# Performance work log

Measured on AMD Instinct MI355X. Metric: run time of the kernel, lower is better.

Reference implementation:

```python
import jax, jax.numpy as jnp
import numpy as np
import math

B, DIM, H, W = 4, 96, 64, 64
DIM3 = DIM * 3
DSTATE = 16

def _dwconv(x, w, b):
    # x: (B, d, L); torch Conv1d(k=4, pad=3, groups=d) then slice [:L] == left-pad 3
    y = jax.lax.conv_general_dilated(x, w, (1,), [(3, 0)],
                                     dimension_numbers=('NCH', 'OIH', 'NCH'),
                                     feature_group_count=x.shape[1])
    return y + b[None, :, None]

def _ln(x, g, b):
    m = jnp.mean(x, -1, keepdims=True)
    v = jnp.var(x, -1, keepdims=True)
    return (x - m) * jax.lax.rsqrt(v + 1e-5) * g + b

def _selective_scan(u, delta, A, Bs, Cs, D, z, delta_bias):
    # u, delta, z: (B, d, L); A: (d, N); Bs, Cs: (B, N, L)
    delta = jax.nn.softplus(delta + delta_bias[None, :, None])
    dT, uT = jnp.moveaxis(delta, 2, 0), jnp.moveaxis(u, 2, 0)   # (L, B, d)
    BT, CT = jnp.moveaxis(Bs, 2, 0), jnp.moveaxis(Cs, 2, 0)     # (L, B, N)
    h0 = jnp.zeros((u.shape[0], A.shape[0], A.shape[1]), u.dtype)
    def step(h, inp):
        d_t, u_t, b_t, c_t = inp
        h = jnp.exp(d_t[..., None] * A) * h + (d_t * u_t)[..., None] * b_t[:, None, :]
        return h, jnp.einsum('bdn,bn->bd', h, c_t)
    _, ys = jax.lax.scan(step, h0, (dT, uT, BT, CT))
    y = jnp.moveaxis(ys, 0, 2) + D[None, :, None] * u
    return y * jax.nn.silu(z)

def _sss(x, z_anchor, in_w, conv_w, conv_b, x_w, dt_w, dt_b, Alog, Dp, out_w):
    Bb, C, Hh, Ww = x.shape
    L = Hh * Ww
    r = dt_w.shape[0]
    xf = x.reshape(Bb, C, L).transpose(0, 2, 1) + z_anchor[:, None, :]
    x_in, z_gate = jnp.split(xf @ in_w, 2, axis=-1)
    xc = jax.nn.silu(_dwconv(x_in.transpose(0, 2, 1), conv_w, conv_b))  # (B, di, L)
    xdbl = xc.transpose(0, 2, 1) @ x_w
    dt, Bs, Cs = jnp.split(xdbl, [r, r + DSTATE], axis=-1)
    y = _selective_scan(xc, (dt @ dt_w).transpose(0, 2, 1), -jnp.exp(Alog),
                        Bs.transpose(0, 2, 1), Cs.transpose(0, 2, 1), Dp,
                        z_gate.transpose(0, 2, 1), dt_b)
    return (y.transpose(0, 2, 1) @ out_w).transpose(0, 2, 1).reshape(Bb, C, Hh, Ww)

def _sts(x, K, Q, in_w, conv_w, conv_b, kln_g, kln_b, k_w, k_b, qln_g, qln_b, q_w, q_b,
         dtbc_w, dt_w, dt_b, gate_w, gate_b, Alog, Dp, out_w):
    Bb, C, Hh, Ww = x.shape
    L = Hh * Ww
    r = dt_w.shape[0]
    xf = x.reshape(Bb, C, L).transpose(0, 2, 1)
    xc = jax.nn.silu(_dwconv((xf @ in_w).transpose(0, 2, 1), conv_w, conv_b))  # (B, di, L)
    x_t = xc.transpose(0, 2, 1)
    Kf = K.reshape(Bb, C, L).transpose(0, 2, 1)
    Qf = Q.reshape(Bb, C, L).transpose(0, 2, 1)
    K_p = jax.nn.silu(_ln(Kf, kln_g, kln_b) @ k_w + k_b)
    Q_p = jax.nn.silu(_ln(Qf, qln_g, qln_b) @ q_w + q_b)
    xdbl = jnp.concatenate([x_t, K_p], -1) @ dtbc_w
    dt, Bs, Cs = jnp.split(xdbl, [r, r + DSTATE], axis=-1)
    z_g = (jnp.concatenate([x_t, Q_p], -1) @ gate_w + gate_b).transpose(0, 2, 1)
    y = _selective_scan(xc, (dt @ dt_w).transpose(0, 2, 1), -jnp.exp(Alog),
                        Bs.transpose(0, 2, 1), Cs.transpose(0, 2, 1), Dp, z_g, dt_b)
    return (y.transpose(0, 2, 1) @ out_w).transpose(0, 2, 1).reshape(Bb, C, Hh, Ww)

def setup_inputs():
    key = jax.random.key(0)
    ks = iter(jax.random.split(key, 64))
    def nrm(shape, s=0.02):
        return jax.random.normal(next(ks), shape, jnp.float32) * s
    di, di3 = DIM * 2, DIM3 * 2
    r, r3 = math.ceil(DIM / 16), math.ceil(DIM3 / 16)
    Alog = jnp.log(jnp.tile(jnp.arange(1.0, DSTATE + 1.0, dtype=jnp.float32), (di, 1)))
    Alog3 = jnp.log(jnp.tile(jnp.arange(1.0, DSTATE + 1.0, dtype=jnp.float32), (di3, 1)))
    return dict(
        m_ll=jax.random.normal(next(ks), (B, DIM, H, W), jnp.float32),
        m_high=jax.random.normal(next(ks), (B, DIM3, H, W), jnp.float32),
        z=jax.random.normal(next(ks), (B, DIM), jnp.float32),
        K=jax.random.normal(next(ks), (B, DIM3, H, W), jnp.float32),
        Q=jax.random.normal(next(ks), (B, DIM3, H, W), jnp.float32),
        s_in_w=nrm((DIM, 2 * di)), s_conv_w=nrm((di, 1, 4), 0.2), s_conv_b=nrm((di,)),
        s_x_w=nrm((di, r + 2 * DSTATE)), s_dt_w=nrm((r, di)), s_dt_b=nrm((di,)),
        s_Alog=Alog, s_D=jnp.ones((di,), jnp.float32), s_out_w=nrm((di, DIM)),
        t_in_w=nrm((DIM3, di3)), t_conv_w=nrm((di3, 1, 4), 0.2), t_conv_b=nrm((di3,)),
        t_kln_g=jnp.ones((DIM3,), jnp.float32), t_kln_b=jnp.zeros((DIM3,), jnp.float32),
        t_k_w=nrm((DIM3, di3)), t_k_b=nrm((di3,)),
        t_qln_g=jnp.ones((DIM3,), jnp.float32), t_qln_b=jnp.zeros((DIM3,), jnp.float32),
        t_q_w=nrm((DIM3, di3)), t_q_b=nrm((di3,)),
        t_dtbc_w=nrm((2 * di3, r3 + 2 * DSTATE)), t_dt_w=nrm((r3, di3)), t_dt_b=nrm((di3,)),
        t_gate_w=nrm((2 * di3, di3)), t_gate_b=nrm((di3,)),
        t_Alog=Alog3, t_D=jnp.ones((di3,), jnp.float32), t_out_w=nrm((di3, DIM3)),
    )

def reference(m_ll, m_high, z, K, Q,
              s_in_w, s_conv_w, s_conv_b, s_x_w, s_dt_w, s_dt_b, s_Alog, s_D, s_out_w,
              t_in_w, t_conv_w, t_conv_b, t_kln_g, t_kln_b, t_k_w, t_k_b,
              t_qln_g, t_qln_b, t_q_w, t_q_b, t_dtbc_w, t_dt_w, t_dt_b,
              t_gate_w, t_gate_b, t_Alog, t_D, t_out_w):
    o1 = m_ll + _sss(m_ll, z, s_in_w, s_conv_w, s_conv_b, s_x_w, s_dt_w, s_dt_b, s_Alog, s_D, s_out_w)
    o2 = m_high + _sts(m_high, K, Q, t_in_w, t_conv_w, t_conv_b, t_kln_g, t_kln_b, t_k_w, t_k_b,
                       t_qln_g, t_qln_b, t_q_w, t_q_b, t_dtbc_w, t_dt_w, t_dt_b,
                       t_gate_w, t_gate_b, t_Alog, t_D, t_out_w)
    return (o1, o2)
```

## Files before the change

### kernel.cpp

```cpp
#include <hip/hip_runtime.h>
#include <math.h>

#define L 4096

typedef unsigned short u16;
typedef unsigned int u32;
typedef float f32x4 __attribute__((ext_vector_type(4)));
typedef short s16x8 __attribute__((ext_vector_type(8)));
typedef __attribute__((address_space(3))) unsigned int lds_u32;
typedef __attribute__((address_space(1))) unsigned int glb_u32;

__device__ __forceinline__ float softplus_f(float x) {
  return fmaxf(x, 0.f) + log1pf(__expf(-fabsf(x)));
}
__device__ __forceinline__ float silu_f(float x) {
  return x / (1.f + __expf(-x));
}
__device__ __forceinline__ float bf2f(u16 v) {
  return __uint_as_float(((unsigned)v) << 16);
}
__device__ __forceinline__ u16 f2bf(float f) {
  unsigned u = __float_as_uint(f);
  u += 0x7FFFu + ((u >> 16) & 1u);
  return (u16)(u >> 16);
}

struct WSeg { const float* src; u16* dst; int K, N, Npad; };
struct WAll { WSeg s[8]; };

__global__ __launch_bounds__(256) void wconv_k(WAll wa) {
  const WSeg w = wa.s[blockIdx.z];
  const int nb = blockIdx.x * 32, kb = blockIdx.y * 32;
  if (nb >= w.Npad || kb >= w.K) return;
  __shared__ float t[32][33];
  const int tx = threadIdx.x & 31, ty = threadIdx.x >> 5;
  for (int r = ty; r < 32; r += 8) {
    int k = kb + r, n = nb + tx;
    t[r][tx] = (n < w.N) ? w.src[(size_t)k * w.N + n] : 0.f;
  }
  __syncthreads();
  for (int r = ty; r < 32; r += 8) {
    int n = nb + r;
    w.dst[(size_t)n * w.K + kb + tx] = f2bf(t[tx][r]);
  }
}

struct TSeg { const float *x, *gam, *bet, *bias2; u16* out; int C, doLN; };
struct TPack { TSeg s[4]; };

__global__ __launch_bounds__(256) void trans_pack_k(TPack pk) {
  const TSeg t = pk.s[blockIdx.x >> 9];
  const int local = blockIdx.x & 511;
  const int C = t.C;
  __shared__ float tile[288][33];
  __shared__ float psum[8][32], psq[8][32];
  __shared__ float mm[32], rr[32];
  const int tid = threadIdx.x;
  const int l0 = (local & 127) * 32;
  const int b = local >> 7;
  const int lane32 = tid & 31, row8 = tid >> 5;
  const float* xb = t.x + (size_t)b * C * L + l0;

  for (int c = row8; c < C; c += 8)
    tile[c][lane32] = xb[(size_t)c * L + lane32];
  __syncthreads();

  if (t.doLN) {
    float s = 0.f, sq = 0.f;
    for (int c = row8; c < C; c += 8) {
      float v = tile[c][lane32];
      s += v; sq = fmaf(v, v, sq);
    }
    psum[row8][lane32] = s; psq[row8][lane32] = sq;
    __syncthreads();
    if (row8 == 0) {
      float ts = 0.f, tq = 0.f;
      #pragma unroll
      for (int g = 0; g < 8; ++g) { ts += psum[g][lane32]; tq += psq[g][lane32]; }
      float m = ts / C;
      float var = tq / C - m * m;
      mm[lane32] = m;
      rr[lane32] = rsqrtf(var + 1e-5f);
    }
    __syncthreads();
  }

  u16* ob = t.out + ((size_t)b * L + l0) * C;
  const int total = 32 * C;
  for (int o = tid * 8; o < total; o += 2048) {
    int tt = o / C, c = o % C;
    float m = 0.f, rs = 0.f;
    if (t.doLN) { m = mm[tt]; rs = rr[tt]; }
    union { u16 u[8]; int4 v; } pkv;
    #pragma unroll
    for (int j = 0; j < 8; ++j) {
      float v = tile[c + j][tt];
      if (t.doLN) v = (v - m) * rs * t.gam[c + j] + t.bet[c + j];
      else if (t.bias2) v += t.bias2[b * C + c + j];
      pkv.u[j] = f2bf(v);
    }
    *(int4*)(ob + o) = pkv.v;
  }
}

struct CSeg { const u16* x; const float* w; const float* b; u16* y; int C, nbx; };
struct CPack { CSeg s[2]; int start1; };

__global__ __launch_bounds__(256) void conv_pack_k(CPack pk) {
  const int bid = blockIdx.x;
  const int si = bid >= pk.start1;
  const CSeg q = pk.s[si];
  const int local = si ? bid - pk.start1 : bid;
  const int C = q.C;
  const int c = (local % q.nbx) * 64 + (threadIdx.x & 63);
  const int chunk = (local / q.nbx) * 4 + (threadIdx.x >> 6);
  const int T0 = chunk * 8;
  const float w0 = q.w[c * 4], w1 = q.w[c * 4 + 1], w2 = q.w[c * 4 + 2], w3 = q.w[c * 4 + 3];
  const float bs = q.b[c];
  const bool first = (T0 & (L - 1)) == 0;
  float v[11];
  #pragma unroll
  for (int i = 0; i < 11; ++i) {
    if (i < 3 && first) v[i] = 0.f;
    else v[i] = bf2f(q.x[(size_t)(T0 - 3 + i) * C + c]);
  }
  #pragma unroll
  for (int j = 0; j < 8; ++j) {
    float s = bs + w0 * v[j] + w1 * v[j + 1] + w2 * v[j + 2] + w3 * v[j + 3];
    q.y[(size_t)(T0 + j) * C + c] = f2bf(silu_f(s));
  }
}

struct MSeg {
  const u16 *A0, *A1, *Wt;
  const float *bias, *res;
  float* outF; u16 *outB0, *outB1;
  int K, K1, Nout, ldA, ldo, split, nbx, nwg, epi;
};
struct MPack { MSeg s[4]; int starts[4]; int nseg; };

__global__ __launch_bounds__(256) void mfma_pack_k(MPack pk) {
  const int bid = blockIdx.x;
  int si = 0;
  #pragma unroll
  for (int k = 1; k < 4; ++k)
    if (k < pk.nseg && bid >= pk.starts[k]) si = k;
  const MSeg p = pk.s[si];
  const int wg = bid - pk.starts[si];

  __shared__ u16 lds[16384];
  u16* As0 = lds;
  u16* Bs0 = lds + 8192;
  const int tid = threadIdx.x;
  const int lane = tid & 63;
  const int wid = tid >> 6;
  const int wm = wid >> 1, wn = wid & 1;
  const int newid = (wg & 7) * (p.nwg >> 3) + (wg >> 3);
  const int n0 = (newid % p.nbx) * 128;
  const int m0 = (newid / p.nbx) * 128;
  const int srow = tid & 127;
  const int skc = tid >> 7;
  const int kgrp = lane >> 4, l16 = lane & 15;

  f32x4 acc[4][4];
  #pragma unroll
  for (int i = 0; i < 4; ++i)
    #pragma unroll
    for (int j = 0; j < 4; ++j)
      acc[i][j] = (f32x4){0.f, 0.f, 0.f, 0.f};

  auto stage = [&](int bi, int k0) {
    const u16* Ab = p.A0;
    int kc = k0;
    if (p.A1 && k0 >= p.K1) { Ab = p.A1; kc = k0 - p.K1; }
    const u16* g0 = Ab + (size_t)(m0 + srow) * p.ldA + kc + skc * 8;
    u16* Ad = As0 + bi * 4096;
    __builtin_amdgcn_global_load_lds((const glb_u32*)g0,
        (lds_u32*)(Ad + wid * 512), 16, 0, 0);
    __builtin_amdgcn_global_load_lds((const glb_u32*)(g0 + 16),
        (lds_u32*)(Ad + 2048 + wid * 512), 16, 0, 0);
    const u16* h0 = p.Wt + (size_t)(n0 + srow) * p.K + k0 + skc * 8;
    u16* Bd = Bs0 + bi * 4096;
    __builtin_amdgcn_global_load_lds((const glb_u32*)h0,
        (lds_u32*)(Bd + wid * 512), 16, 0, 0);
    __builtin_amdgcn_global_load_lds((const glb_u32*)(h0 + 16),
        (lds_u32*)(Bd + 2048 + wid * 512), 16, 0, 0);
  };

  const int nt = p.K >> 5;
  stage(0, 0);
  __syncthreads();
  for (int t = 0; t < nt; ++t) {
    const int cur = t & 1;
    if (t + 1 < nt) stage(cur ^ 1, (t + 1) << 5);
    s16x8 af[4], bfr[4];
    #pragma unroll
    for (int mi = 0; mi < 4; ++mi)
      af[mi] = *(const s16x8*)(As0 + cur * 4096 + kgrp * 1024 + (wm * 64 + mi * 16 + l16) * 8);
    #pragma unroll
    for (int ni = 0; ni < 4; ++ni)
      bfr[ni] = *(const s16x8*)(Bs0 + cur * 4096 + kgrp * 1024 + (wn * 64 + ni * 16 + l16) * 8);
    #pragma unroll
    for (int mi = 0; mi < 4; ++mi)
      #pragma unroll
      for (int ni = 0; ni < 4; ++ni)
        acc[mi][ni] = __builtin_amdgcn_mfma_f32_16x16x32_bf16(af[mi], bfr[ni], acc[mi][ni], 0, 0, 0);
    if (t + 1 < nt) __syncthreads();
  }

  if (p.epi == 0) {
    #pragma unroll
    for (int mi = 0; mi < 4; ++mi) {
      #pragma unroll
      for (int j = 0; j < 4; ++j) {
        int token = m0 + wm * 64 + mi * 16 + (lane >> 4) * 4 + j;
        #pragma unroll
        for (int ni = 0; ni < 4; ++ni) {
          int n = n0 + wn * 64 + ni * 16 + l16;
          if (n < p.Nout) p.outF[(size_t)token * p.ldo + n] = acc[mi][ni][j];
        }
      }
    }
  } else if (p.epi == 2) {
    #pragma unroll
    for (int mi = 0; mi < 4; ++mi) {
      int token = m0 + wm * 64 + mi * 16 + (lane >> 4) * 4;
      int b = token >> 12, l = token & (L - 1);
      #pragma unroll
      for (int ni = 0; ni < 4; ++ni) {
        int n = n0 + wn * 64 + ni * 16 + l16;
        if (n < p.Nout) {
          size_t o = ((size_t)b * p.Nout + n) * L + l;
          float4 r = *(const float4*)(p.res + o);
          float4 v = make_float4(acc[mi][ni][0] + r.x, acc[mi][ni][1] + r.y,
                                 acc[mi][ni][2] + r.z, acc[mi][ni][3] + r.w);
          *(float4*)(p.outF + o) = v;
        }
      }
    }
  } else {
    __syncthreads();
    #pragma unroll
    for (int mi = 0; mi < 4; ++mi) {
      #pragma unroll
      for (int j = 0; j < 4; ++j) {
        int tok = wm * 64 + mi * 16 + (lane >> 4) * 4 + j;
        #pragma unroll
        for (int ni = 0; ni < 4; ++ni) {
          int nl = wn * 64 + ni * 16 + l16;
          int n = n0 + nl;
          float v = acc[mi][ni][j];
          if (n < p.Nout && (p.epi == 3 || p.epi == 4)) {
            v += p.bias[n];
            if (p.epi == 3) v = silu_f(v);
          }
          lds[tok * 128 + ((((nl >> 4) ^ (tok & 7))) << 4) + (nl & 15)] = f2bf(v);
        }
      }
    }
    __syncthreads();
    #pragma unroll
    for (int it = 0; it < 8; ++it) {
      int idx = it * 256 + tid;
      int row = idx >> 4, c16 = idx & 15;
      int nl0 = c16 * 8;
      if (n0 + nl0 < p.Nout) {
        int g = nl0 >> 4;
        int4 vv = *(const int4*)(lds + row * 128 + ((g ^ (row & 7)) << 4) + (nl0 & 15));
        int token = m0 + row;
        if (p.epi == 5) {
          int n = n0 + nl0;
          if (n < p.split) *(int4*)(p.outB0 + (size_t)token * p.split + n) = vv;
          else *(int4*)(p.outB1 + (size_t)token * p.split + (n - p.split)) = vv;
        } else {
          *(int4*)(p.outB0 + (size_t)token * p.ldo + n0 + nl0) = vv;
        }
      }
    }
  }
}

struct FSeg { const float* A0; const float* W; const float* eb; float* out; int K, N, lda, ldo, nbx; };
struct FPack { FSeg s[2]; int start1; };

__global__ __launch_bounds__(256) void gemm_f32_pack_k(FPack pk) {
  const int bid = blockIdx.x;
  const int si = bid >= pk.start1;
  const FSeg p = pk.s[si];
  const int local = si ? bid - pk.start1 : bid;
  const int n0 = (local % p.nbx) * 64;
  const int m0 = (local / p.nbx) * 64;

  __shared__ __align__(16) float As[16][64];
  __shared__ __align__(16) float Bs[16][64];
  const int tid = threadIdx.x;
  const int kidx = tid >> 4;
  const int li4 = (tid & 15) << 2;
  const int r0 = (tid & 15) << 2;
  const int c0 = (tid >> 4) << 2;
  float acc[4][4] = {};

  for (int k0 = 0; k0 < p.K; k0 += 16) {
    __syncthreads();
    {
      const int row = tid >> 2;
      const int kk4 = (tid & 3) << 2;
      const float* src = p.A0 + (size_t)(m0 + row) * p.lda;
      #pragma unroll
      for (int j = 0; j < 4; ++j) {
        int k = k0 + kk4 + j;
        As[kk4 + j][row] = (k < p.K) ? src[k] : 0.f;
      }
    }
    {
      int k = k0 + kidx;
      #pragma unroll
      for (int j = 0; j < 4; ++j) {
        int n = n0 + li4 + j;
        Bs[kidx][li4 + j] = (k < p.K && n < p.N) ? p.W[(size_t)k * p.N + n] : 0.f;
      }
    }
    __syncthreads();
    #pragma unroll
    for (int kk = 0; kk < 16; ++kk) {
      float4 a = *(const float4*)&As[kk][r0];
      float4 bq = *(const float4*)&Bs[kk][c0];
      float av[4] = {a.x, a.y, a.z, a.w};
      float bv[4] = {bq.x, bq.y, bq.z, bq.w};
      #pragma unroll
      for (int i = 0; i < 4; ++i)
        #pragma unroll
        for (int j = 0; j < 4; ++j)
          acc[i][j] = fmaf(av[i], bv[j], acc[i][j]);
    }
  }
  float eb[4] = {p.eb[n0 + c0], p.eb[n0 + c0 + 1], p.eb[n0 + c0 + 2], p.eb[n0 + c0 + 3]};
  #pragma unroll
  for (int i = 0; i < 4; ++i) {
    float4 v;
    v.x = softplus_f(acc[i][0] + eb[0]);
    v.y = softplus_f(acc[i][1] + eb[1]);
    v.z = softplus_f(acc[i][2] + eb[2]);
    v.w = softplus_f(acc[i][3] + eb[3]);
    *(float4*)&p.out[(size_t)(m0 + r0 + i) * p.ldo + n0 + c0] = v;
  }
}

struct S3Seg {
  const u16* u; const float* dlt; const float* Alog; const float* xdbl;
  const float* Dp; const u16* zT; float* PF; float* PF2; u16* yT;
  int roff, Dch, CLen, NCH, nsl, cSplit;
};
struct S3Pack { S3Seg s[2]; int start1; };

template<int PASS>
__global__ __launch_bounds__(256) void scan3_pack_k(S3Pack pk) {
  __shared__ float rows[64][32];
  const int bid = blockIdx.x;
  const int si = bid >= pk.start1;
  const S3Seg q = pk.s[si];
  const int local = si ? bid - pk.start1 : bid;
  const int nsl = q.nsl;
  const int NC = L / q.CLen;
  const int slice = local % nsl;
  const int c = (local / nsl) % NC;
  const int b = local / (nsl * NC);
  const int tid = threadIdx.x;
  const size_t tok0 = (size_t)b * L + (size_t)c * q.CLen;

  float* PFb;
  int cc;
  if (c < q.cSplit) { PFb = q.PF; cc = c; }
  else { PFb = q.PF2; cc = c - q.cSplit; }

  const int W2 = (PASS == 1) ? 8 : 16;
  const int tot2 = q.CLen * W2;
  for (int i = tid; i < tot2; i += 256) {
    int r = i / W2, j = i - r * W2;
    float2 v = *(const float2*)(q.xdbl + (tok0 + r) * 64 + q.roff + 2 * j);
    *(float2*)&rows[r][2 * j] = v;
  }
  __syncthreads();

  if (tid < 192) {
    const int d = slice * 192 + tid;
    const int Dch = q.Dch;
    float An[16], h[16];
    #pragma unroll
    for (int n = 0; n < 16; ++n) {
      An[n] = -__expf(q.Alog[d * 16 + n]);
      h[n] = 0.f;
    }
    bool fast = true;
    #pragma unroll
    for (int n = 1; n < 16; ++n) {
      float ref = (float)(n + 1) * An[0];
      if (fabsf(An[n] - ref) > 1e-4f * fabsf(ref)) fast = false;
    }
    const int ch = b * Dch + d;
    if (PASS == 3) {
      #pragma unroll
      for (int n = 0; n < 16; ++n)
        h[n] = PFb[((size_t)cc * 32 + 16 + n) * q.NCH + ch];
    }
    const float Dd = q.Dp[d];
    const u16* up = q.u + tok0 * Dch + d;
    const float* dp = q.dlt + tok0 * Dch + d;
    const u16* zp = q.zT + tok0 * Dch + d;
    u16* yr = q.yT + tok0 * Dch + d;
    float S = 0.f;

    #define SCAN_BODY(FAST)                                                    \
    for (int t = 0; t < q.CLen; ++t) {                                         \
      const size_t od = (size_t)t * Dch;                                       \
      float dl = dp[od];                                                       \
      float uu = bf2f(up[od]);                                                 \
      float w = dl * uu;                                                       \
      f32x4 B4[4];                                                             \
      _Pragma("unroll")                                                        \
      for (int g = 0; g < 4; ++g) B4[g] = *(const f32x4*)&rows[t][4 * g];      \
      if (PASS == 1) S += dl;                                                  \
      float y = 0.f;                                                           \
      if (FAST) {                                                              \
        float a = __expf(dl * An[0]);                                          \
        float e = a;                                                           \
        h[0] = fmaf(e, h[0], w * B4[0][0]);                                    \
        _Pragma("unroll")                                                      \
        for (int n = 1; n < 16; ++n) {                                         \
          e *= a;                                                              \
          h[n] = fmaf(e, h[n], w * B4[n >> 2][n & 3]);                         \
        }                                                                      \
      } else {                                                                 \
        _Pragma("unroll")                                                      \
        for (int n = 0; n < 16; ++n)                                           \
          h[n] = fmaf(__expf(dl * An[n]), h[n], w * B4[n >> 2][n & 3]);        \
      }                                                                        \
      if (PASS == 3) {                                                         \
        f32x4 C4[4];                                                           \
        _Pragma("unroll")                                                      \
        for (int g = 0; g < 4; ++g) C4[g] = *(const f32x4*)&rows[t][16 + 4 * g]; \
        _Pragma("unroll")                                                      \
        for (int n = 0; n < 16; ++n)                                           \
          y = fmaf(h[n], C4[n >> 2][n & 3], y);                                \
        float zv = bf2f(zp[od]);                                               \
        yr[od] = f2bf((y + Dd * uu) * silu_f(zv));                             \
      }                                                                        \
    }

    if (fast) { SCAN_BODY(1) } else { SCAN_BODY(0) }
    #undef SCAN_BODY

    if (PASS == 1) {
      #pragma unroll
      for (int n = 0; n < 16; ++n) {
        PFb[((size_t)cc * 32 + n) * q.NCH + ch] = __expf(An[n] * S);
        PFb[((size_t)cc * 32 + 16 + n) * q.NCH + ch] = h[n];
      }
    }
  }
}

__global__ __launch_bounds__(256) void stitch_pack_k(
    float* PA0, float* PB0, int sp0, int NC0, int NCH0, int tot0,
    float* PA1, float* PB1, int sp1, int NC1, int NCH1, int tot1) {
  int idx = blockIdx.x * 256 + threadIdx.x;
  float *PA, *PB; int sp, NC, NCH;
  if (idx < tot0) { PA = PA0; PB = PB0; sp = sp0; NC = NC0; NCH = NCH0; }
  else { idx -= tot0; if (idx >= tot1) return; PA = PA1; PB = PB1; sp = sp1; NC = NC1; NCH = NCH1; }
  int ch = idx % NCH, n = idx / NCH;
  float hin = 0.f;
  for (int c = 0; c < NC; ++c) {
    float* base = (c < sp) ? PA : PB;
    int cc = (c < sp) ? c : c - sp;
    float* Ps = base + ((size_t)cc * 32 + n) * NCH + ch;
    float* Fs = base + ((size_t)cc * 32 + 16 + n) * NCH + ch;
    float Pv = *Ps, Fv = *Fs;
    *Fs = hin;
    hin = fmaf(Pv, hin, Fv);
  }
}

extern "C" void kernel_launch(void* const* d_in, const int* in_sizes, int n_in,
                              void* d_out, int out_size, void* d_ws, size_t ws_size,
                              hipStream_t stream) {
  const float* m_ll    = (const float*)d_in[0];
  const float* m_high  = (const float*)d_in[1];
  const float* zanc    = (const float*)d_in[2];
  const float* Kin     = (const float*)d_in[3];
  const float* Qin     = (const float*)d_in[4];
  const float* s_in_w  = (const float*)d_in[5];
  const float* s_conv_w= (const float*)d_in[6];
  const float* s_conv_b= (const float*)d_in[7];
  const float* s_x_w   = (const float*)d_in[8];
  const float* s_dt_w  = (const float*)d_in[9];
  const float* s_dt_b  = (const float*)d_in[10];
  const float* s_Alog  = (const float*)d_in[11];
  const float* s_D     = (const float*)d_in[12];
  const float* s_out_w = (const float*)d_in[13];
  const float* t_in_w  = (const float*)d_in[14];
  const float* t_conv_w= (const float*)d_in[15];
  const float* t_conv_b= (const float*)d_in[16];
  const float* t_kln_g = (const float*)d_in[17];
  const float* t_kln_b = (const float*)d_in[18];
  const float* t_k_w   = (const float*)d_in[19];
  const float* t_k_b   = (const float*)d_in[20];
  const float* t_qln_g = (const float*)d_in[21];
  const float* t_qln_b = (const float*)d_in[22];
  const float* t_q_w   = (const float*)d_in[23];
  const float* t_q_b   = (const float*)d_in[24];
  const float* t_dtbc_w= (const float*)d_in[25];
  const float* t_dt_w  = (const float*)d_in[26];
  const float* t_dt_b  = (const float*)d_in[27];
  const float* t_gate_w= (const float*)d_in[28];
  const float* t_gate_b= (const float*)d_in[29];
  const float* t_Alog  = (const float*)d_in[30];
  const float* t_D     = (const float*)d_in[31];
  const float* t_out_w = (const float*)d_in[32];

  float* out1 = (float*)d_out;
  float* out2 = out1 + (size_t)4 * 96 * L;
  float* ws = (float*)d_ws;

  u16* w_sin   = (u16*)(ws + 0);
  u16* w_sx    = (u16*)(ws + 18432);
  u16* w_sout  = (u16*)(ws + 30720);
  u16* w_tin   = (u16*)(ws + 43008);
  u16* w_tk    = (u16*)(ws + 135168);
  u16* w_tq    = (u16*)(ws + 227328);
  u16* w_tdtbc = (u16*)(ws + 319488);
  u16* w_tgate = (u16*)(ws + 393216);
  u16* w_tout  = (u16*)(ws + 761856);

  float* B_ahi  = ws + 872448;
  float* B_aK   = ws + 3231744;
  float* B_aQ   = ws + 5591040;
  float* B_all  = ws + 7950336;
  float* B_xin  = ws + 8736768;
  float* B_zTs  = ws + 10309632;
  float* B_xc   = ws + 11882496;
  float* B_xin3 = ws + 13455360;
  float* B_xc3  = ws + 18173952;
  float* B_kp   = ws + 22892544;
  float* B_qp   = ws + 27611136;
  float* B_zg3  = ws + 32329728;
  float* B_xdbl = ws + 37048320;
  float* B_xdbl3= ws + 38096896;
  float* B_PFs  = ws + 39145472;
  float* B_dlt  = B_ahi;
  float* B_dlt3 = B_kp;
  u16* y_bf = (u16*)B_xin;
  u16* y3   = (u16*)B_xin3;
  float* PFt_a = out2;
  float* PFt_b = ws + 4018176;

  dim3 blk(256);

  {
    WAll wa;
    wa.s[0] = {s_in_w,   w_sin,    96, 384, 384};
    wa.s[1] = {s_x_w,    w_sx,    192,  38, 128};
    wa.s[2] = {s_out_w,  w_sout,  192,  96, 128};
    wa.s[3] = {t_in_w,   w_tin,   288, 576, 640};
    wa.s[4] = {t_k_w,    w_tk,    288, 576, 640};
    wa.s[5] = {t_q_w,    w_tq,    288, 576, 640};
    wa.s[6] = {t_dtbc_w, w_tdtbc, 1152, 50, 128};
    wa.s[7] = {t_gate_w, w_tgate, 1152, 576, 640};
    wconv_k<<<dim3(20, 36, 8), blk, 0, stream>>>(wa);
    WAll wb;
    wb.s[0] = {t_out_w,  w_tout,  576, 288, 384};
    wconv_k<<<dim3(12, 18, 1), blk, 0, stream>>>(wb);
  }

  {
    TPack tp{};
    tp.s[0] = {m_ll,   nullptr, nullptr, zanc,    (u16*)B_all, 96,  0};
    tp.s[1] = {m_high, nullptr, nullptr, nullptr, (u16*)B_ahi, 288, 0};
    tp.s[2] = {Kin,    t_kln_g, t_kln_b, nullptr, (u16*)B_aK,  288, 1};
    tp.s[3] = {Qin,    t_qln_g, t_qln_b, nullptr, (u16*)B_aQ,  288, 1};
    trans_pack_k<<<dim3(2048), blk, 0, stream>>>(tp);
  }

  {
    MPack pk{}; pk.nseg = 4;
    pk.starts[0] = 0; pk.starts[1] = 384; pk.starts[2] = 1024; pk.starts[3] = 1664;
    MSeg a{}; a.A0 = (u16*)B_all; a.Wt = w_sin; a.K = 96; a.K1 = 1 << 28; a.Nout = 384;
    a.ldA = 96; a.split = 192; a.outB0 = (u16*)B_xin; a.outB1 = (u16*)B_zTs;
    a.nbx = 3; a.nwg = 384; a.epi = 5; pk.s[0] = a;
    MSeg b{}; b.A0 = (u16*)B_ahi; b.Wt = w_tin; b.K = 288; b.K1 = 1 << 28; b.Nout = 576;
    b.ldA = 288; b.ldo = 576; b.outB0 = (u16*)B_xin3; b.nbx = 5; b.nwg = 640; b.epi = 1; pk.s[1] = b;
    MSeg c{}; c.A0 = (u16*)B_aK; c.Wt = w_tk; c.K = 288; c.K1 = 1 << 28; c.Nout = 576;
    c.ldA = 288; c.ldo = 576; c.bias = t_k_b; c.outB0 = (u16*)B_kp; c.nbx = 5; c.nwg = 640; c.epi = 3; pk.s[2] = c;
    MSeg d{}; d.A0 = (u16*)B_aQ; d.Wt = w_tq; d.K = 288; d.K1 = 1 << 28; d.Nout = 576;
    d.ldA = 288; d.ldo = 576; d.bias = t_q_b; d.outB0 = (u16*)B_qp; d.nbx = 5; d.nwg = 640; d.epi = 3; pk.s[3] = d;
    mfma_pack_k<<<dim3(2304), blk, 0, stream>>>(pk);
  }

  {
    CPack cp{}; cp.start1 = 1536;
    cp.s[0] = {(u16*)B_xin,  s_conv_w, s_conv_b, (u16*)B_xc,  192, 3};
    cp.s[1] = {(u16*)B_xin3, t_conv_w, t_conv_b, (u16*)B_xc3, 576, 9};
    conv_pack_k<<<dim3(6144), blk, 0, stream>>>(cp);
  }

  {
    MPack pk{}; pk.nseg = 3;
    pk.starts[0] = 0; pk.starts[1] = 128; pk.starts[2] = 256; pk.starts[3] = 896;
    MSeg a{}; a.A0 = (u16*)B_xc; a.Wt = w_sx; a.K = 192; a.K1 = 1 << 28; a.Nout = 64;
    a.ldA = 192; a.ldo = 64; a.outF = B_xdbl; a.nbx = 1; a.nwg = 128; a.epi = 0; pk.s[0] = a;
    MSeg b{}; b.A0 = (u16*)B_xc3; b.A1 = (u16*)B_kp; b.Wt = w_tdtbc; b.K = 1152; b.K1 = 576;
    b.Nout = 64; b.ldA = 576; b.ldo = 64; b.outF = B_xdbl3; b.nbx = 1; b.nwg = 128; b.epi = 0; pk.s[1] = b;
    MSeg c{}; c.A0 = (u16*)B_xc3; c.A1 = (u16*)B_qp; c.Wt = w_tgate; c.K = 1152; c.K1 = 576;
    c.Nout = 576; c.ldA = 576; c.ldo = 576; c.bias = t_gate_b; c.outB0 = (u16*)B_zg3;
    c.nbx = 5; c.nwg = 640; c.epi = 4; pk.s[2] = c;
    mfma_pack_k<<<dim3(896), blk, 0, stream>>>(pk);
  }

  {
    FPack fp{}; fp.start1 = 768;
    fp.s[0] = {B_xdbl,  s_dt_w, s_dt_b, B_dlt,  6,  192, 64, 192, 3};
    fp.s[1] = {B_xdbl3, t_dt_w, t_dt_b, B_dlt3, 18, 576, 64, 576, 9};
    gemm_f32_pack_k<<<dim3(3072), blk, 0, stream>>>(fp);
  }

  S3Pack sp{}; sp.start1 = 512;
  sp.s[0] = {(u16*)B_xc,  B_dlt,  s_Alog, B_xdbl,  s_D, (u16*)B_zTs, B_PFs, B_PFs, y_bf, 6,  192, 32, 768,  1, 128};
  sp.s[1] = {(u16*)B_xc3, B_dlt3, t_Alog, B_xdbl3, t_D, (u16*)B_zg3, PFt_a, PFt_b, y3,   18, 576, 32, 2304, 3, 64};
  scan3_pack_k<1><<<dim3(2048), blk, 0, stream>>>(sp);
  stitch_pack_k<<<dim3(192), blk, 0, stream>>>(
      B_PFs, B_PFs, 128, 128, 768, 12288,
      PFt_a, PFt_b, 64, 128, 2304, 36864);
  scan3_pack_k<3><<<dim3(2048), blk, 0, stream>>>(sp);

  {
    MPack pk{}; pk.nseg = 2;
    pk.starts[0] = 0; pk.starts[1] = 128; pk.starts[2] = 512; pk.starts[3] = 512;
    MSeg a{}; a.A0 = y_bf; a.Wt = w_sout; a.K = 192; a.K1 = 1 << 28; a.Nout = 96;
    a.ldA = 192; a.res = m_ll; a.outF = out1; a.nbx = 1; a.nwg = 128; a.epi = 2; pk.s[0] = a;
    MSeg b{}; b.A0 = y3; b.Wt = w_tout; b.K = 576; b.K1 = 1 << 28; b.Nout = 288;
    b.ldA = 576; b.res = m_high; b.outF = out2; b.nbx = 3; b.nwg = 384; b.epi = 2; pk.s[1] = b;
    mfma_pack_k<<<dim3(512), blk, 0, stream>>>(pk);
  }
}
```

Measured before the change: 390.1 us.

## Fuse dt projection and softplus into x_proj MFMA epilogue, drop f32 GEMM

The separate fp32 GEMM that projected dt (rank 6/18) to d_inner channels and applied softplus is removed. Instead, the x_proj MFMA kernel stages its 128x64 output tile in LDS and computes the dt projection plus bias and softplus per channel in a new epilogue, writing delta directly. Workspace buffers are reshuffled so delta and scan prefix buffers get new locations, with split pointers for the second batch half. This removes one launch and a round trip of xdbl through global memory, but adds a serial 128-token loop per channel in the epilogue, which may lengthen those blocks.

```diff
diff --git a/kernel.cpp b/kernel.cpp
--- a/kernel.cpp
+++ b/kernel.cpp
@@ -134,8 +134,10 @@
 struct MSeg {
   const u16 *A0, *A1, *Wt;
   const float *bias, *res;
-  float* outF; u16 *outB0, *outB1;
-  int K, K1, Nout, ldA, ldo, split, nbx, nwg, epi;
+  const float *dtw2, *dtb2;
+  float *outF, *dltOut, *dltOut2;
+  u16 *outB0, *outB1;
+  int K, K1, Nout, ldA, ldo, split, nbx, nwg, epi, rdim, DchOut, dltSplitTok;
 };
 struct MPack { MSeg s[4]; int starts[4]; int nseg; };
 
@@ -208,7 +210,7 @@
     if (t + 1 < nt) __syncthreads();
   }
 
-  if (p.epi == 0) {
+  if (p.epi == 0 || p.epi == 6) {
     #pragma unroll
     for (int mi = 0; mi < 4; ++mi) {
       #pragma unroll
@@ -218,6 +220,41 @@
         for (int ni = 0; ni < 4; ++ni) {
           int n = n0 + wn * 64 + ni * 16 + l16;
           if (n < p.Nout) p.outF[(size_t)token * p.ldo + n] = acc[mi][ni][j];
+        }
+      }
+    }
+    if (p.epi == 6) {
+      __syncthreads();
+      float* ldsf = (float*)lds;
+      #pragma unroll
+      for (int mi = 0; mi < 4; ++mi) {
+        #pragma unroll
+        for (int j = 0; j < 4; ++j) {
+          int tok = wm * 64 + mi * 16 + (lane >> 4) * 4 + j;
+          #pragma unroll
+          for (int ni = 0; ni < 4; ++ni) {
+            int nl = wn * 64 + ni * 16 + l16;
+            if (nl < 64) ldsf[tok * 64 + nl] = acc[mi][ni][j];
+          }
+        }
+      }
+      __syncthreads();
+      float* dbase;
+      int moff;
+      if (m0 < p.dltSplitTok) { dbase = p.dltOut; moff = m0; }
+      else { dbase = p.dltOut2; moff = m0 - p.dltSplitTok; }
+      for (int ch = tid; ch < p.DchOut; ch += 256) {
+        float wc[18];
+        #pragma unroll
+        for (int k = 0; k < 18; ++k)
+          wc[k] = (k < p.rdim) ? p.dtw2[k * p.DchOut + ch] : 0.f;
+        const float db = p.dtb2[ch];
+        for (int tok = 0; tok < 128; ++tok) {
+          float a0 = db;
+          #pragma unroll
+          for (int k = 0; k < 18; ++k)
+            a0 = fmaf(ldsf[tok * 64 + k], wc[k], a0);
+          dbase[(size_t)(moff + tok) * p.DchOut + ch] = softplus_f(a0);
         }
       }
     }
@@ -280,76 +317,11 @@
   }
 }
 
-struct FSeg { const float* A0; const float* W; const float* eb; float* out; int K, N, lda, ldo, nbx; };
-struct FPack { FSeg s[2]; int start1; };
-
-__global__ __launch_bounds__(256) void gemm_f32_pack_k(FPack pk) {
-  const int bid = blockIdx.x;
-  const int si = bid >= pk.start1;
-  const FSeg p = pk.s[si];
-  const int local = si ? bid - pk.start1 : bid;
-  const int n0 = (local % p.nbx) * 64;
-  const int m0 = (local / p.nbx) * 64;
-
-  __shared__ __align__(16) float As[16][64];
-  __shared__ __align__(16) float Bs[16][64];
-  const int tid = threadIdx.x;
-  const int kidx = tid >> 4;
-  const int li4 = (tid & 15) << 2;
-  const int r0 = (tid & 15) << 2;
-  const int c0 = (tid >> 4) << 2;
-  float acc[4][4] = {};
-
-  for (int k0 = 0; k0 < p.K; k0 += 16) {
-    __syncthreads();
-    {
-      const int row = tid >> 2;
-      const int kk4 = (tid & 3) << 2;
-      const float* src = p.A0 + (size_t)(m0 + row) * p.lda;
-      #pragma unroll
-      for (int j = 0; j < 4; ++j) {
-        int k = k0 + kk4 + j;
-        As[kk4 + j][row] = (k < p.K) ? src[k] : 0.f;
-      }
-    }
-    {
-      int k = k0 + kidx;
-      #pragma unroll
-      for (int j = 0; j < 4; ++j) {
-        int n = n0 + li4 + j;
-        Bs[kidx][li4 + j] = (k < p.K && n < p.N) ? p.W[(size_t)k * p.N + n] : 0.f;
-      }
-    }
-    __syncthreads();
-    #pragma unroll
-    for (int kk = 0; kk < 16; ++kk) {
-      float4 a = *(const float4*)&As[kk][r0];
-      float4 bq = *(const float4*)&Bs[kk][c0];
-      float av[4] = {a.x, a.y, a.z, a.w};
-      float bv[4] = {bq.x, bq.y, bq.z, bq.w};
-      #pragma unroll
-      for (int i = 0; i < 4; ++i)
-        #pragma unroll
-        for (int j = 0; j < 4; ++j)
-          acc[i][j] = fmaf(av[i], bv[j], acc[i][j]);
-    }
-  }
-  float eb[4] = {p.eb[n0 + c0], p.eb[n0 + c0 + 1], p.eb[n0 + c0 + 2], p.eb[n0 + c0 + 3]};
-  #pragma unroll
-  for (int i = 0; i < 4; ++i) {
-    float4 v;
-    v.x = softplus_f(acc[i][0] + eb[0]);
-    v.y = softplus_f(acc[i][1] + eb[1]);
-    v.z = softplus_f(acc[i][2] + eb[2]);
-    v.w = softplus_f(acc[i][3] + eb[3]);
-    *(float4*)&p.out[(size_t)(m0 + r0 + i) * p.ldo + n0 + c0] = v;
-  }
-}
-
 struct S3Seg {
-  const u16* u; const float* dlt; const float* Alog; const float* xdbl;
-  const float* Dp; const u16* zT; float* PF; float* PF2; u16* yT;
-  int roff, Dch, CLen, NCH, nsl, cSplit;
+  const u16* u; const float* dlt; const float* dlt2; const float* Alog;
+  const float* xdbl; const float* Dp; const u16* zT; float* PF; float* PF2;
+  u16* yT;
+  int roff, Dch, CLen, NCH, nsl, cSplit, bSplit;
 };
 struct S3Pack { S3Seg s[2]; int start1; };
 
@@ -372,6 +344,10 @@
   int cc;
   if (c < q.cSplit) { PFb = q.PF; cc = c; }
   else { PFb = q.PF2; cc = c - q.cSplit; }
+  const float* dltb;
+  size_t dtok;
+  if (b < q.bSplit) { dltb = q.dlt; dtok = tok0; }
+  else { dltb = q.dlt2; dtok = tok0 - (size_t)q.bSplit * L; }
 
   const int W2 = (PASS == 1) ? 8 : 16;
   const int tot2 = q.CLen * W2;
@@ -405,7 +381,7 @@
     }
     const float Dd = q.Dp[d];
     const u16* up = q.u + tok0 * Dch + d;
-    const float* dp = q.dlt + tok0 * Dch + d;
+    const float* dp = dltb + dtok * Dch + d;
     const u16* zp = q.zT + tok0 * Dch + d;
     u16* yr = q.yT + tok0 * Dch + d;
     float S = 0.f;
@@ -546,12 +522,12 @@
   float* B_xdbl = ws + 37048320;
   float* B_xdbl3= ws + 38096896;
   float* B_PFs  = ws + 39145472;
-  float* B_dlt  = B_ahi;
-  float* B_dlt3 = B_kp;
+  float* D3A   = out2;
+  float* D3B   = ws + 872448;
+  float* DLT_S = ws + 5591040;
+  float* PF_T  = B_kp;
   u16* y_bf = (u16*)B_xin;
   u16* y3   = (u16*)B_xin3;
-  float* PFt_a = out2;
-  float* PFt_b = ws + 4018176;
 
   dim3 blk(256);
 
@@ -606,29 +582,26 @@
     MPack pk{}; pk.nseg = 3;
     pk.starts[0] = 0; pk.starts[1] = 128; pk.starts[2] = 256; pk.starts[3] = 896;
     MSeg a{}; a.A0 = (u16*)B_xc; a.Wt = w_sx; a.K = 192; a.K1 = 1 << 28; a.Nout = 64;
-    a.ldA = 192; a.ldo = 64; a.outF = B_xdbl; a.nbx = 1; a.nwg = 128; a.epi = 0; pk.s[0] = a;
+    a.ldA = 192; a.ldo = 64; a.outF = B_xdbl; a.nbx = 1; a.nwg = 128; a.epi = 6;
+    a.dtw2 = s_dt_w; a.dtb2 = s_dt_b; a.dltOut = DLT_S; a.dltOut2 = DLT_S;
+    a.rdim = 6; a.DchOut = 192; a.dltSplitTok = 1 << 28; pk.s[0] = a;
     MSeg b{}; b.A0 = (u16*)B_xc3; b.A1 = (u16*)B_kp; b.Wt = w_tdtbc; b.K = 1152; b.K1 = 576;
-    b.Nout = 64; b.ldA = 576; b.ldo = 64; b.outF = B_xdbl3; b.nbx = 1; b.nwg = 128; b.epi = 0; pk.s[1] = b;
+    b.Nout = 64; b.ldA = 576; b.ldo = 64; b.outF = B_xdbl3; b.nbx = 1; b.nwg = 128; b.epi = 6;
+    b.dtw2 = t_dt_w; b.dtb2 = t_dt_b; b.dltOut = D3A; b.dltOut2 = D3B;
+    b.rdim = 18; b.DchOut = 576; b.dltSplitTok = 8192; pk.s[1] = b;
     MSeg c{}; c.A0 = (u16*)B_xc3; c.A1 = (u16*)B_qp; c.Wt = w_tgate; c.K = 1152; c.K1 = 576;
     c.Nout = 576; c.ldA = 576; c.ldo = 576; c.bias = t_gate_b; c.outB0 = (u16*)B_zg3;
     c.nbx = 5; c.nwg = 640; c.epi = 4; pk.s[2] = c;
     mfma_pack_k<<<dim3(896), blk, 0, stream>>>(pk);
   }
 
-  {
-    FPack fp{}; fp.start1 = 768;
-    fp.s[0] = {B_xdbl,  s_dt_w, s_dt_b, B_dlt,  6,  192, 64, 192, 3};
-    fp.s[1] = {B_xdbl3, t_dt_w, t_dt_b, B_dlt3, 18, 576, 64, 576, 9};
-    gemm_f32_pack_k<<<dim3(3072), blk, 0, stream>>>(fp);
-  }
-
   S3Pack sp{}; sp.start1 = 512;
-  sp.s[0] = {(u16*)B_xc,  B_dlt,  s_Alog, B_xdbl,  s_D, (u16*)B_zTs, B_PFs, B_PFs, y_bf, 6,  192, 32, 768,  1, 128};
-  sp.s[1] = {(u16*)B_xc3, B_dlt3, t_Alog, B_xdbl3, t_D, (u16*)B_zg3, PFt_a, PFt_b, y3,   18, 576, 32, 2304, 3, 64};
+  sp.s[0] = {(u16*)B_xc,  DLT_S, DLT_S, s_Alog, B_xdbl,  s_D, (u16*)B_zTs, B_PFs, B_PFs, y_bf, 6,  192, 32, 768,  1, 128, 4};
+  sp.s[1] = {(u16*)B_xc3, D3A,   D3B,   t_Alog, B_xdbl3, t_D, (u16*)B_zg3, PF_T,  PF_T,  y3,   18, 576, 32, 2304, 3, 128, 2};
   scan3_pack_k<1><<<dim3(2048), blk, 0, stream>>>(sp);
   stitch_pack_k<<<dim3(192), blk, 0, stream>>>(
       B_PFs, B_PFs, 128, 128, 768, 12288,
-      PFt_a, PFt_b, 64, 128, 2304, 36864);
+      PF_T,  PF_T,  128, 128, 2304, 36864);
   scan3_pack_k<3><<<dim3(2048), blk, 0, stream>>>(sp);
 
   {
```

After: 448.4 us. +15.0%, slower.
